# Kernel tuning notes

Measured on AMD Instinct MI355X. Metric: run time of the kernel, lower is better.

The kernel has to match this reference:

```python
import jax, jax.numpy as jnp
import numpy as np

D = 512
E = 1024
LAMBDA_INIT = 0.05

def setup_inputs() -> dict:
    key = jax.random.key(0)
    ks = jax.random.split(key, 8)
    B, S = 4, 4096
    X = jax.random.normal(ks[0], (B, S, E), dtype=jnp.float32)
    Wq = jax.random.normal(ks[1], (2 * D, E), dtype=jnp.float32) / np.sqrt(E)
    bq = jnp.zeros((2 * D,), dtype=jnp.float32)
    Wk = jax.random.normal(ks[2], (2 * D, E), dtype=jnp.float32) / np.sqrt(E)
    bk = jnp.zeros((2 * D,), dtype=jnp.float32)
    Wv = jax.random.normal(ks[3], (D, E), dtype=jnp.float32) / np.sqrt(E)
    bv = jnp.zeros((D,), dtype=jnp.float32)
    lam = jax.random.normal(ks[4], (1,), dtype=jnp.float32)
    return {"X": X, "Wq": Wq, "bq": bq, "Wk": Wk, "bk": bk, "Wv": Wv, "bv": bv, "lam": lam}

def reference(X, Wq, bq, Wk, bk, Wv, bv, lam):
    # Linear projections (torch Linear: x @ W.T + b)
    Q = jnp.einsum('bse,fe->bsf', X, Wq) + bq   # [B,S,2d]
    K = jnp.einsum('bse,fe->bsf', X, Wk) + bk   # [B,S,2d]
    V = jnp.einsum('bse,de->bsd', X, Wv) + bv   # [B,S,d]
    Q1, Q2 = Q[..., :D], Q[..., D:]
    K1, K2 = K[..., :D], K[..., D:]
    s = 1.0 / np.sqrt(D)
    A1 = jnp.einsum('bqd,bkd->bqk', Q1, K1) * s  # [B,S,S]
    A2 = jnp.einsum('bqd,bkd->bqk', Q2, K2) * s
    P1 = jax.nn.softmax(A1, axis=-1)
    P2 = jax.nn.softmax(A2, axis=-1)
    lambda_ = jnp.exp(lam) + LAMBDA_INIT         # scalar [1]
    diff = P1 - lambda_ * P2
    return jnp.einsum('bqk,bkd->bqd', diff, V)   # [B,S,d]
```

## Files before the change

kernel.cpp:

```cpp
#include <hip/hip_runtime.h>
#include <cstdint>
#include <cstddef>

#define NB    4
#define SEQ   4096
#define EDIM  1024
#define DHEAD 512
#define NTOK  (NB * SEQ)
#define FQK   2048
#define FQKV  2560

typedef __bf16 bf16x8 __attribute__((ext_vector_type(8)));
typedef float  f32x4  __attribute__((ext_vector_type(4)));

__device__ __forceinline__ unsigned short f2bf(float f) {
  union { float f; unsigned int u; } v; v.f = f;
  return (unsigned short)((v.u + 0x7fffu + ((v.u >> 16) & 1u)) >> 16);
}
__device__ __forceinline__ float bf2f(unsigned short h) {
  union { unsigned int u; float f; } v; v.u = ((unsigned int)h) << 16;
  return v.f;
}

__device__ __forceinline__ void gld_lds16(const void* g, void* l) {
  __builtin_amdgcn_global_load_lds(
      (const __attribute__((address_space(1))) unsigned int*)g,
      (__attribute__((address_space(3))) unsigned int*)l, 16, 0, 0);
}

template <class Epi>
__device__ __forceinline__ void gemm_bt_core(
    const unsigned short* __restrict__ A, const unsigned short* __restrict__ B,
    int K, int lda, int ldb, int m0, int n0, Epi epi) {
  __shared__ __align__(16) unsigned short As[128 * 32];
  __shared__ __align__(16) unsigned short Bs[128 * 32];
  const int t = threadIdx.x;
  const int w = t >> 6;
  const int lane = t & 63;
  const int wr = w >> 1, wc = w & 1;

  f32x4 acc[4][4];
#pragma unroll
  for (int i = 0; i < 4; ++i)
#pragma unroll
    for (int j = 0; j < 4; ++j) acc[i][j] = f32x4{0.f, 0.f, 0.f, 0.f};

  const int c0 = (w * 2) * 64 + lane;
  const int c1 = (w * 2 + 1) * 64 + lane;
  const int r0 = c0 >> 2, col0 = (c0 & 3) * 8;
  const int r1 = c1 >> 2, col1 = (c1 & 3) * 8;
  unsigned short* ldsA0 = &As[(w * 2) * 512];
  unsigned short* ldsA1 = &As[(w * 2 + 1) * 512];
  unsigned short* ldsB0 = &Bs[(w * 2) * 512];
  unsigned short* ldsB1 = &Bs[(w * 2 + 1) * 512];
  const unsigned short* gA0 = A + (size_t)(m0 + r0) * lda + col0;
  const unsigned short* gA1 = A + (size_t)(m0 + r1) * lda + col1;
  const unsigned short* gB0 = B + (size_t)(n0 + r0) * ldb + col0;
  const unsigned short* gB1 = B + (size_t)(n0 + r1) * ldb + col1;

  for (int kt = 0; kt < K; kt += 32) {
    gld_lds16(gA0 + kt, ldsA0);
    gld_lds16(gA1 + kt, ldsA1);
    gld_lds16(gB0 + kt, ldsB0);
    gld_lds16(gB1 + kt, ldsB1);
    __syncthreads();

    bf16x8 af[4], bfr[4];
#pragma unroll
    for (int tm = 0; tm < 4; ++tm) {
      int r = wr * 64 + tm * 16 + (lane & 15);
      af[tm] = *(const bf16x8*)&As[r * 32 + (lane >> 4) * 8];
    }
#pragma unroll
    for (int tn = 0; tn < 4; ++tn) {
      int r = wc * 64 + tn * 16 + (lane & 15);
      bfr[tn] = *(const bf16x8*)&Bs[r * 32 + (lane >> 4) * 8];
    }
#pragma unroll
    for (int tm = 0; tm < 4; ++tm)
#pragma unroll
      for (int tn = 0; tn < 4; ++tn)
        acc[tm][tn] = __builtin_amdgcn_mfma_f32_16x16x32_bf16(
            af[tm], bfr[tn], acc[tm][tn], 0, 0, 0);
    __syncthreads();
  }
  epi(acc, wr, wc, lane);
}

__global__ void k_cvt_x(const float* __restrict__ X, unsigned short* __restrict__ Xb) {
  int i = blockIdx.x * blockDim.x + threadIdx.x;
  float4 v = ((const float4*)X)[i];
  ushort4 o;
  o.x = f2bf(v.x); o.y = f2bf(v.y); o.z = f2bf(v.z); o.w = f2bf(v.w);
  ((ushort4*)Xb)[i] = o;
}

__global__ void k_pack_w(const float* __restrict__ Wq, const float* __restrict__ Wk,
                         const float* __restrict__ Wv, unsigned short* __restrict__ Wb) {
  int i = blockIdx.x * blockDim.x + threadIdx.x;
  int idx = i * 4;
  int f = idx >> 10, e = idx & 1023;
  const float* src = (f < 1024) ? (Wq + (size_t)f * 1024)
                   : (f < 2048) ? (Wk + (size_t)(f - 1024) * 1024)
                                : (Wv + (size_t)(f - 2048) * 1024);
  float4 v = *(const float4*)(src + e);
  ushort4 o;
  o.x = f2bf(v.x); o.y = f2bf(v.y); o.z = f2bf(v.z); o.w = f2bf(v.w);
  ((ushort4*)Wb)[i] = o;
}

__global__ void k_pack_b(const float* __restrict__ bq, const float* __restrict__ bk,
                         const float* __restrict__ bv, float* __restrict__ bc) {
  int f = blockIdx.x * blockDim.x + threadIdx.x;
  if (f < FQKV)
    bc[f] = (f < 1024) ? bq[f] : (f < 2048) ? bk[f - 1024] : bv[f - 2048];
}

__global__ void k_zero_f(float* __restrict__ p) {
  int i = blockIdx.x * blockDim.x + threadIdx.x;
  p[i] = 0.f;
}

__global__ __launch_bounds__(256) void k_qk(const unsigned short* __restrict__ Xb,
                                            const unsigned short* __restrict__ Wb,
                                            const float* __restrict__ bc,
                                            unsigned short* __restrict__ QK) {
  __shared__ __align__(16) unsigned short Ps[128 * 136];
  const int m0 = blockIdx.y * 128, n0 = blockIdx.x * 128;
  gemm_bt_core(Xb, Wb, EDIM, EDIM, EDIM, m0, n0,
    [&](f32x4 (&acc)[4][4], int wr, int wc, int lane) {
      const int w = wr * 2 + wc;
#pragma unroll
      for (int tm = 0; tm < 4; ++tm)
#pragma unroll
        for (int tn = 0; tn < 4; ++tn) {
          int kc = wc * 64 + tn * 16 + (lane & 15);
          float bias = bc[n0 + kc];
#pragma unroll
          for (int i = 0; i < 4; ++i) {
            int ql = wr * 64 + tm * 16 + (lane >> 4) * 4 + i;
            Ps[ql * 136 + kc] = f2bf(acc[tm][tn][i] + bias);
          }
        }
      __syncthreads();
#pragma unroll
      for (int j = 0; j < 8; ++j) {
        int row = w * 32 + j * 4 + (lane >> 4);
        int col = (lane & 15) * 8;
        uint4 v = *(const uint4*)&Ps[row * 136 + col];
        *(uint4*)&QK[(size_t)(m0 + row) * FQK + n0 + col] = v;
      }
    });
}

__global__ __launch_bounds__(256) void k_v(const unsigned short* __restrict__ Xb,
                                           const unsigned short* __restrict__ Wb,
                                           const float* __restrict__ bc,
                                           unsigned short* __restrict__ Vt) {
  const int b = blockIdx.z;
  const int m0 = blockIdx.y * 128;
  const int n0 = blockIdx.x * 128;
  const unsigned short* A = Wb + (size_t)2048 * EDIM;
  const unsigned short* B = Xb + (size_t)b * SEQ * EDIM;
  unsigned short* Vb = Vt + (size_t)b * DHEAD * SEQ;
  gemm_bt_core(A, B, EDIM, EDIM, EDIM, m0, n0,
    [&](f32x4 (&acc)[4][4], int wr, int wc, int lane) {
#pragma unroll
      for (int tm = 0; tm < 4; ++tm)
#pragma unroll
        for (int tn = 0; tn < 4; ++tn) {
          int s = n0 + wc * 64 + tn * 16 + (lane & 15);
#pragma unroll
          for (int i = 0; i < 4; ++i) {
            int d = m0 + wr * 64 + tm * 16 + (lane >> 4) * 4 + i;
            Vb[(size_t)d * SEQ + s] = f2bf(acc[tm][tn][i] + bc[2048 + d]);
          }
        }
    });
}

__global__ __launch_bounds__(256) void k_scores2(const unsigned short* __restrict__ QK,
                                                 unsigned short* __restrict__ E_c,
                                                 float* __restrict__ ls, int b0) {
  __shared__ __align__(16) unsigned short Ps[128 * 136];
  const int z = blockIdx.z;
  const int rb = z >> 1, which = z & 1;
  const int b = b0 + rb;
  const int m0 = blockIdx.y * 128;
  const int n0 = blockIdx.x * 128;
  const unsigned short* Aq = QK + (size_t)b * SEQ * FQK + which * 512;
  const unsigned short* Bk = QK + (size_t)b * SEQ * FQK + 1024 + which * 512;
  unsigned short* Eb = E_c + (size_t)z * SEQ * SEQ;
  float* lr = ls + (size_t)which * NTOK + (size_t)b * SEQ;
  gemm_bt_core(Aq, Bk, 512, FQK, FQK, m0, n0,
    [&](f32x4 (&acc)[4][4], int wr, int wc, int lane) {
      const float scale = 0.04419417382415922f;
      const int w = wr * 2 + wc;
      float rs[4][4];
#pragma unroll
      for (int tm = 0; tm < 4; ++tm)
#pragma unroll
        for (int i = 0; i < 4; ++i) rs[tm][i] = 0.f;
#pragma unroll
      for (int tm = 0; tm < 4; ++tm)
#pragma unroll
        for (int tn = 0; tn < 4; ++tn) {
          int kc = wc * 64 + tn * 16 + (lane & 15);
#pragma unroll
          for (int i = 0; i < 4; ++i) {
            int ql = wr * 64 + tm * 16 + (lane >> 4) * 4 + i;
            float e = __expf(acc[tm][tn][i] * scale);
            unsigned short eb = f2bf(e);
            Ps[ql * 136 + kc] = eb;
            rs[tm][i] += bf2f(eb);
          }
        }
#pragma unroll
      for (int tm = 0; tm < 4; ++tm)
#pragma unroll
        for (int i = 0; i < 4; ++i) {
          float v = rs[tm][i];
          v += __shfl_xor(v, 1);
          v += __shfl_xor(v, 2);
          v += __shfl_xor(v, 4);
          v += __shfl_xor(v, 8);
          rs[tm][i] = v;
        }
      if ((lane & 15) == 0) {
#pragma unroll
        for (int tm = 0; tm < 4; ++tm)
#pragma unroll
          for (int i = 0; i < 4; ++i) {
            int q = m0 + wr * 64 + tm * 16 + (lane >> 4) * 4 + i;
            atomicAdd(&lr[q], rs[tm][i]);
          }
      }
      __syncthreads();
#pragma unroll
      for (int j = 0; j < 8; ++j) {
        int row = w * 32 + j * 4 + (lane >> 4);
        int col = (lane & 15) * 8;
        uint4 v = *(const uint4*)&Ps[row * 136 + col];
        *(uint4*)&Eb[(size_t)(m0 + row) * SEQ + n0 + col] = v;
      }
    });
}

__global__ __launch_bounds__(256) void k_pv4(const unsigned short* __restrict__ E_c,
                                             const unsigned short* __restrict__ Vt,
                                             float* __restrict__ O12, int b0) {
  __shared__ __align__(16) unsigned short As[64 * 32];
  __shared__ __align__(16) unsigned short Bs[256 * 32];
  const int bid = blockIdx.x;
  const int z = (bid >> 1) & 3;
  const int e = (bid & 1) | ((bid >> 3) << 1);
  const int q0 = (e >> 1) * 64;
  const int n0 = (e & 1) * 256;
  const int b = b0 + (z >> 1);
  const unsigned short* A = E_c + (size_t)z * SEQ * SEQ;
  const unsigned short* Bv = Vt + (size_t)b * DHEAD * SEQ;
  float* Ob = O12 + (size_t)z * SEQ * DHEAD;
  const int t = threadIdx.x, w = t >> 6, lane = t & 63;

  f32x4 acc[4][4];
#pragma unroll
  for (int i = 0; i < 4; ++i)
#pragma unroll
    for (int j = 0; j < 4; ++j) acc[i][j] = f32x4{0.f, 0.f, 0.f, 0.f};

  const int ca = w * 64 + lane;
  const unsigned short* gA = A + (size_t)(q0 + (ca >> 2)) * SEQ + (ca & 3) * 8;
  unsigned short* ldsA = As + (w * 64) * 8;
  const unsigned short* gB[4];
  unsigned short* ldsB[4];
#pragma unroll
  for (int g = 0; g < 4; ++g) {
    int c = w * 256 + g * 64 + lane;
    gB[g] = Bv + (size_t)(n0 + (c >> 2)) * SEQ + (c & 3) * 8;
    ldsB[g] = Bs + (w * 256 + g * 64) * 8;
  }

  for (int kt = 0; kt < SEQ; kt += 32) {
    gld_lds16(gA + kt, ldsA);
#pragma unroll
    for (int g = 0; g < 4; ++g) gld_lds16(gB[g] + kt, ldsB[g]);
    __syncthreads();

    bf16x8 af[4], bfr[4];
#pragma unroll
    for (int tm = 0; tm < 4; ++tm) {
      int r = tm * 16 + (lane & 15);
      af[tm] = *(const bf16x8*)&As[r * 32 + (lane >> 4) * 8];
    }
#pragma unroll
    for (int tn = 0; tn < 4; ++tn) {
      int r = w * 64 + tn * 16 + (lane & 15);
      bfr[tn] = *(const bf16x8*)&Bs[r * 32 + (lane >> 4) * 8];
    }
#pragma unroll
    for (int tm = 0; tm < 4; ++tm)
#pragma unroll
      for (int tn = 0; tn < 4; ++tn)
        acc[tm][tn] = __builtin_amdgcn_mfma_f32_16x16x32_bf16(
            af[tm], bfr[tn], acc[tm][tn], 0, 0, 0);
    __syncthreads();
  }

#pragma unroll
  for (int tm = 0; tm < 4; ++tm)
#pragma unroll
    for (int tn = 0; tn < 4; ++tn) {
      int d = n0 + w * 64 + tn * 16 + (lane & 15);
#pragma unroll
      for (int i = 0; i < 4; ++i) {
        int q = q0 + tm * 16 + (lane >> 4) * 4 + i;
        Ob[(size_t)q * DHEAD + d] = acc[tm][tn][i];
      }
    }
}

__global__ void k_combine(const float* __restrict__ O12, const float* __restrict__ ls,
                          const float* __restrict__ lam, float* __restrict__ out, int b0) {
  int i = blockIdx.x * blockDim.x + threadIdx.x;
  float lambda = expf(lam[0]) + 0.05f;
  int gq = i >> 7;
  int rb = gq >> 12;
  int q = gq & 4095;
  int dv = i & 127;
  int b = b0 + rb;
  float inv1 = 1.f / ls[(size_t)b * SEQ + q];
  float inv2 = lambda / ls[NTOK + (size_t)b * SEQ + q];
  size_t ai = (size_t)(rb * 2) * (SEQ * 128) + (size_t)q * 128 + dv;
  float4 a = ((const float4*)O12)[ai];
  float4 c = ((const float4*)O12)[ai + SEQ * 128];
  float4 r;
  r.x = a.x * inv1 - c.x * inv2;
  r.y = a.y * inv1 - c.y * inv2;
  r.z = a.z * inv1 - c.z * inv2;
  r.w = a.w * inv1 - c.w * inv2;
  ((float4*)out)[(size_t)(b * SEQ + q) * 128 + dv] = r;
}

extern "C" void kernel_launch(void* const* d_in, const int* in_sizes, int n_in,
                              void* d_out, int out_size, void* d_ws, size_t ws_size,
                              hipStream_t stream) {
  const float* X   = (const float*)d_in[0];
  const float* Wq  = (const float*)d_in[1];
  const float* bq  = (const float*)d_in[2];
  const float* Wk  = (const float*)d_in[3];
  const float* bk  = (const float*)d_in[4];
  const float* Wv  = (const float*)d_in[5];
  const float* bv  = (const float*)d_in[6];
  const float* lam = (const float*)d_in[7];
  float* out = (float*)d_out;

  char* ws = (char*)d_ws;
  size_t off = 0;
  auto alloc = [&](size_t b) { size_t r = off; off += (b + 255) & ~(size_t)255; return r; };
  unsigned short* Xb  = (unsigned short*)(ws + alloc((size_t)NTOK * EDIM * 2));
  unsigned short* Wb  = (unsigned short*)(ws + alloc((size_t)FQKV * EDIM * 2));
  float*          bc  = (float*)(ws + alloc((size_t)FQKV * 4));
  unsigned short* QK  = (unsigned short*)(ws + alloc((size_t)NTOK * FQK * 2));
  unsigned short* Vt  = (unsigned short*)(ws + alloc((size_t)NB * DHEAD * SEQ * 2));
  unsigned short* E_c = (unsigned short*)(ws + alloc((size_t)4 * SEQ * SEQ * 2));
  float*          ls  = (float*)(ws + alloc((size_t)2 * NTOK * 4));
  float* O12 = (float*)Xb;

  k_cvt_x<<<dim3((NTOK * EDIM / 4) / 256), dim3(256), 0, stream>>>(X, Xb);
  k_pack_w<<<dim3((FQKV * EDIM / 4) / 256), dim3(256), 0, stream>>>(Wq, Wk, Wv, Wb);
  k_pack_b<<<dim3(10), dim3(256), 0, stream>>>(bq, bk, bv, bc);
  k_qk<<<dim3(FQK / 128, NTOK / 128), dim3(256), 0, stream>>>(Xb, Wb, bc, QK);
  k_v<<<dim3(SEQ / 128, DHEAD / 128, NB), dim3(256), 0, stream>>>(Xb, Wb, bc, Vt);
  k_zero_f<<<dim3(2 * NTOK / 256), dim3(256), 0, stream>>>(ls);
  for (int b0 = 0; b0 < NB; b0 += 2) {
    k_scores2<<<dim3(SEQ / 128, SEQ / 128, 4), dim3(256), 0, stream>>>(QK, E_c, ls, b0);
    k_pv4<<<dim3(512), dim3(256), 0, stream>>>(E_c, Vt, O12, b0);
    k_combine<<<dim3((2 * SEQ * DHEAD / 4) / 256), dim3(256), 0, stream>>>(O12, ls, lam, out, b0);
  }

  (void)in_sizes; (void)n_in; (void)out_size; (void)ws_size;
}
```

Before: 763.5 us.

## Enlarge score tile to 256x128 with 8 waves and direct global stores

Replaces the scores kernel with an inline 512-thread kernel computing 256x128 tiles, doubling reuse of each K tile. The epilogue writes the exponentiated bf16 scores directly to global memory instead of staging them through LDS for 16-byte vector stores. This is meant to cut LDS traffic and the extra barrier, at the cost of narrower, less coalesced global stores and a simple single-buffered K loop.

After: 732.6 us. -4.1%, faster.

```diff
diff --git a/kernel.cpp b/kernel.cpp
--- a/kernel.cpp
+++ b/kernel.cpp
@@ -179,71 +179,105 @@
     });
 }
 
-__global__ __launch_bounds__(256) void k_scores2(const unsigned short* __restrict__ QK,
+__global__ __launch_bounds__(512) void k_scores3(const unsigned short* __restrict__ QK,
                                                  unsigned short* __restrict__ E_c,
                                                  float* __restrict__ ls, int b0) {
-  __shared__ __align__(16) unsigned short Ps[128 * 136];
+  __shared__ __align__(16) unsigned short As[256 * 32];
+  __shared__ __align__(16) unsigned short Bs[128 * 32];
   const int z = blockIdx.z;
   const int rb = z >> 1, which = z & 1;
   const int b = b0 + rb;
-  const int m0 = blockIdx.y * 128;
+  const int m0 = blockIdx.y * 256;
   const int n0 = blockIdx.x * 128;
   const unsigned short* Aq = QK + (size_t)b * SEQ * FQK + which * 512;
   const unsigned short* Bk = QK + (size_t)b * SEQ * FQK + 1024 + which * 512;
   unsigned short* Eb = E_c + (size_t)z * SEQ * SEQ;
   float* lr = ls + (size_t)which * NTOK + (size_t)b * SEQ;
-  gemm_bt_core(Aq, Bk, 512, FQK, FQK, m0, n0,
-    [&](f32x4 (&acc)[4][4], int wr, int wc, int lane) {
-      const float scale = 0.04419417382415922f;
-      const int w = wr * 2 + wc;
-      float rs[4][4];
-#pragma unroll
-      for (int tm = 0; tm < 4; ++tm)
-#pragma unroll
-        for (int i = 0; i < 4; ++i) rs[tm][i] = 0.f;
-#pragma unroll
-      for (int tm = 0; tm < 4; ++tm)
-#pragma unroll
-        for (int tn = 0; tn < 4; ++tn) {
-          int kc = wc * 64 + tn * 16 + (lane & 15);
-#pragma unroll
-          for (int i = 0; i < 4; ++i) {
-            int ql = wr * 64 + tm * 16 + (lane >> 4) * 4 + i;
-            float e = __expf(acc[tm][tn][i] * scale);
-            unsigned short eb = f2bf(e);
-            Ps[ql * 136 + kc] = eb;
-            rs[tm][i] += bf2f(eb);
-          }
-        }
-#pragma unroll
-      for (int tm = 0; tm < 4; ++tm)
-#pragma unroll
-        for (int i = 0; i < 4; ++i) {
-          float v = rs[tm][i];
-          v += __shfl_xor(v, 1);
-          v += __shfl_xor(v, 2);
-          v += __shfl_xor(v, 4);
-          v += __shfl_xor(v, 8);
-          rs[tm][i] = v;
-        }
-      if ((lane & 15) == 0) {
-#pragma unroll
-        for (int tm = 0; tm < 4; ++tm)
-#pragma unroll
-          for (int i = 0; i < 4; ++i) {
-            int q = m0 + wr * 64 + tm * 16 + (lane >> 4) * 4 + i;
-            atomicAdd(&lr[q], rs[tm][i]);
-          }
+  const int t = threadIdx.x, w = t >> 6, lane = t & 63;
+  const int wr = w >> 1, wc = w & 1;
+
+  f32x4 acc[4][4];
+#pragma unroll
+  for (int i = 0; i < 4; ++i)
+#pragma unroll
+    for (int j = 0; j < 4; ++j) acc[i][j] = f32x4{0.f, 0.f, 0.f, 0.f};
+
+  const int cA0 = w * 128 + lane;
+  const int cA1 = w * 128 + 64 + lane;
+  const int cB  = w * 64 + lane;
+  const unsigned short* gA0 = Aq + (size_t)(m0 + (cA0 >> 2)) * FQK + (cA0 & 3) * 8;
+  const unsigned short* gA1 = Aq + (size_t)(m0 + (cA1 >> 2)) * FQK + (cA1 & 3) * 8;
+  const unsigned short* gB  = Bk + (size_t)(n0 + (cB >> 2)) * FQK + (cB & 3) * 8;
+  unsigned short* ldsA0 = As + (w * 128) * 8;
+  unsigned short* ldsA1 = As + (w * 128 + 64) * 8;
+  unsigned short* ldsB  = Bs + (w * 64) * 8;
+
+  for (int kt = 0; kt < 512; kt += 32) {
+    gld_lds16(gA0 + kt, ldsA0);
+    gld_lds16(gA1 + kt, ldsA1);
+    gld_lds16(gB + kt, ldsB);
+    __syncthreads();
+
+    bf16x8 af[4], bfr[4];
+#pragma unroll
+    for (int tm = 0; tm < 4; ++tm) {
+      int r = wr * 64 + tm * 16 + (lane & 15);
+      af[tm] = *(const bf16x8*)&As[r * 32 + (lane >> 4) * 8];
+    }
+#pragma unroll
+    for (int tn = 0; tn < 4; ++tn) {
+      int r = wc * 64 + tn * 16 + (lane & 15);
+      bfr[tn] = *(const bf16x8*)&Bs[r * 32 + (lane >> 4) * 8];
+    }
+#pragma unroll
+    for (int tm = 0; tm < 4; ++tm)
+#pragma unroll
+      for (int tn = 0; tn < 4; ++tn)
+        acc[tm][tn] = __builtin_amdgcn_mfma_f32_16x16x32_bf16(
+            af[tm], bfr[tn], acc[tm][tn], 0, 0, 0);
+    __syncthreads();
+  }
+
+  const float scale = 0.04419417382415922f;
+  float rs[4][4];
+#pragma unroll
+  for (int tm = 0; tm < 4; ++tm)
+#pragma unroll
+    for (int i = 0; i < 4; ++i) rs[tm][i] = 0.f;
+#pragma unroll
+  for (int tm = 0; tm < 4; ++tm)
+#pragma unroll
+    for (int tn = 0; tn < 4; ++tn) {
+      int k = n0 + wc * 64 + tn * 16 + (lane & 15);
+#pragma unroll
+      for (int i = 0; i < 4; ++i) {
+        int q = m0 + wr * 64 + tm * 16 + (lane >> 4) * 4 + i;
+        float e = __expf(acc[tm][tn][i] * scale);
+        unsigned short eb = f2bf(e);
+        Eb[(size_t)q * SEQ + k] = eb;
+        rs[tm][i] += bf2f(eb);
       }
-      __syncthreads();
-#pragma unroll
-      for (int j = 0; j < 8; ++j) {
-        int row = w * 32 + j * 4 + (lane >> 4);
-        int col = (lane & 15) * 8;
-        uint4 v = *(const uint4*)&Ps[row * 136 + col];
-        *(uint4*)&Eb[(size_t)(m0 + row) * SEQ + n0 + col] = v;
+    }
+#pragma unroll
+  for (int tm = 0; tm < 4; ++tm)
+#pragma unroll
+    for (int i = 0; i < 4; ++i) {
+      float v = rs[tm][i];
+      v += __shfl_xor(v, 1);
+      v += __shfl_xor(v, 2);
+      v += __shfl_xor(v, 4);
+      v += __shfl_xor(v, 8);
+      rs[tm][i] = v;
+    }
+  if ((lane & 15) == 0) {
+#pragma unroll
+    for (int tm = 0; tm < 4; ++tm)
+#pragma unroll
+      for (int i = 0; i < 4; ++i) {
+        int q = m0 + wr * 64 + tm * 16 + (lane >> 4) * 4 + i;
+        atomicAdd(&lr[q], rs[tm][i]);
       }
-    });
+  }
 }
 
 __global__ __launch_bounds__(256) void k_pv4(const unsigned short* __restrict__ E_c,
@@ -373,7 +407,7 @@
   k_v<<<dim3(SEQ / 128, DHEAD / 128, NB), dim3(256), 0, stream>>>(Xb, Wb, bc, Vt);
   k_zero_f<<<dim3(2 * NTOK / 256), dim3(256), 0, stream>>>(ls);
   for (int b0 = 0; b0 < NB; b0 += 2) {
-    k_scores2<<<dim3(SEQ / 128, SEQ / 128, 4), dim3(256), 0, stream>>>(QK, E_c, ls, b0);
+    k_scores3<<<dim3(SEQ / 128, SEQ / 256, 4), dim3(512), 0, stream>>>(QK, E_c, ls, b0);
     k_pv4<<<dim3(512), dim3(256), 0, stream>>>(E_c, Vt, O12, b0);
     k_combine<<<dim3((2 * SEQ * DHEAD / 4) / 256), dim3(256), 0, stream>>>(O12, ls, lam, out, b0);
   }
```
